# Optimization experiments

Measured on AMD Instinct MI355X. Metric: run time of the kernel, lower is better.

Reference implementation:

```python
import jax, jax.numpy as jnp
import numpy as np

DIM = 128
N_NODES = 100000
N_EDGES = 200000
M = 800000  # incidence pairs in each direction
L = 2
N_CLASS = 10


def setup_inputs() -> dict:
    key = jax.random.key(0)
    ks = jax.random.split(key, 8)
    s = 1.0 / np.sqrt(DIM)
    return {
        "node_x": jax.random.normal(ks[0], (N_NODES, DIM), jnp.float32),
        "nodes_map": jax.random.randint(ks[1], (M,), 0, N_NODES, jnp.int32),
        "edge_seg": jnp.sort(jax.random.randint(ks[2], (M,), 0, N_EDGES, jnp.int32)),
        "edges_map": jax.random.randint(ks[3], (M,), 0, N_EDGES, jnp.int32),
        "node_seg": jnp.sort(jax.random.randint(ks[4], (M,), 0, N_NODES, jnp.int32)),
        "num_edges": N_EDGES,
        "W_e": jax.random.normal(ks[5], (L, DIM, DIM), jnp.float32) * s,
        "b_e": jnp.zeros((L, DIM), jnp.float32),
        "g_e": jnp.ones((L, DIM), jnp.float32),
        "be_e": jnp.zeros((L, DIM), jnp.float32),
        "W_n": jax.random.normal(ks[6], (L, DIM, DIM), jnp.float32) * s,
        "b_n": jnp.zeros((L, DIM), jnp.float32),
        "g_n": jnp.ones((L, DIM), jnp.float32),
        "be_n": jnp.zeros((L, DIM), jnp.float32),
        "W_c": jax.random.normal(ks[7], (DIM, N_CLASS), jnp.float32) * s,
        "b_c": jnp.zeros((N_CLASS,), jnp.float32),
    }


def _seg_mean(x, seg, num_segments):
    # global_mean_pool: segment sum / count (count clamped to 1 for empty segments)
    s = jax.ops.segment_sum(x, seg, num_segments=num_segments)
    cnt = jax.ops.segment_sum(jnp.ones((x.shape[0],), x.dtype), seg, num_segments=num_segments)
    return s / jnp.maximum(cnt, 1.0)[:, None]


def _layernorm(x, g, b, eps=1e-5):
    m = jnp.mean(x, axis=-1, keepdims=True)
    v = jnp.mean(jnp.square(x - m), axis=-1, keepdims=True)
    return (x - m) * jax.lax.rsqrt(v + eps) * g + b


def reference(node_x, nodes_map, edge_seg, edges_map, node_seg, num_edges,
              W_e, b_e, g_e, be_e, W_n, b_n, g_n, be_n, W_c, b_c):
    n_nodes = node_x.shape[0]
    x = node_x  # in_drp = Dropout(0.0) is identity
    for i in range(W_e.shape[0]):
        # N2E: gather node feats per (edge, member) pair, mean-pool per hyperedge
        ex = _seg_mean(x[nodes_map], edge_seg, num_edges)          # [E, DIM]
        ex = jax.nn.relu(_layernorm(ex @ W_e[i] + b_e[i], g_e[i], be_e[i]))
        # E2N: gather edge feats per (node, incident-edge) pair, mean-pool per node
        x = _seg_mean(ex[edges_map], node_seg, n_nodes)            # [N, DIM]
        x = jax.nn.relu(_layernorm(x @ W_n[i] + b_n[i], g_n[i], be_n[i]))
    return jax.nn.log_softmax(x @ W_c + b_c, axis=-1)
```

## Files before the change

### kernel.cpp

```cpp
#include <hip/hip_runtime.h>
#include <hip/hip_bf16.h>

#define DIM 128

typedef __bf16 bf16x8 __attribute__((ext_vector_type(8)));
typedef float f32x4 __attribute__((ext_vector_type(4)));

static inline int cdiv(int a, int b) { return (a + b - 1) / b; }
static inline size_t align256(size_t x) { return (x + 255) & ~size_t(255); }

__device__ inline unsigned short f2bf(float f) {
    union { float f; unsigned int u; } v; v.f = f;
    unsigned int r = v.u + 0x7fff + ((v.u >> 16) & 1);
    return (unsigned short)(r >> 16);
}
__device__ inline unsigned int hb(float f) {
    return (__builtin_bit_cast(unsigned int, f) + 0x8000u) >> 16;
}

__global__ void setup_all_kernel(const int* __restrict__ segA, int mA, int nA,
                                 int* __restrict__ offA,
                                 const int* __restrict__ segB, int mB, int nB,
                                 int* __restrict__ offB,
                                 const float* __restrict__ xin,
                                 unsigned short* __restrict__ xout, int n4,
                                 const float* __restrict__ W_e,
                                 const float* __restrict__ W_n,
                                 unsigned short* __restrict__ wsw) {
    int gid = blockIdx.x * blockDim.x + threadIdx.x;

    if (gid < n4) {
        float4 v = ((const float4*)xin)[gid];
        ushort4 o;
        o.x = f2bf(v.x); o.y = f2bf(v.y); o.z = f2bf(v.z); o.w = f2bf(v.w);
        ((ushort4*)xout)[gid] = o;
    }

    if (gid <= nA) {
        int lo = 0, hi = mA;
        while (lo < hi) { int mid = (lo + hi) >> 1; if (segA[mid] < gid) lo = mid + 1; else hi = mid; }
        offA[gid] = lo;
    }
    int jj = gid - (nA + 1);
    if (jj >= 0 && jj <= nB) {
        int lo = 0, hi = mB;
        while (lo < hi) { int mid = (lo + hi) >> 1; if (segB[mid] < jj) lo = mid + 1; else hi = mid; }
        offB[jj] = lo;
    }

    if (gid < 8192) {
        int mi = gid >> 11;
        int e = gid & 2047;
        const float* W = (mi < 2) ? (W_e + (size_t)mi * DIM * DIM)
                                  : (W_n + (size_t)(mi - 2) * DIM * DIM);
        int t = e >> 9, n = (e >> 6) & 7, lane = e & 63;
        int q = lane >> 4, c = lane & 15;
        int k0 = t * 32 + q * 8, col = n * 16 + c;
        unsigned short vals[8];
#pragma unroll
        for (int j = 0; j < 8; ++j) vals[j] = f2bf(W[(size_t)(k0 + j) * DIM + col]);
        ushort4* dst = (ushort4*)(wsw + (size_t)gid * 8);
        dst[0] = make_ushort4(vals[0], vals[1], vals[2], vals[3]);
        dst[1] = make_ushort4(vals[4], vals[5], vals[6], vals[7]);
    }
}

__device__ inline void accum8(float* a, uint4 v) {
    unsigned int u[4] = {v.x, v.y, v.z, v.w};
#pragma unroll
    for (int i = 0; i < 4; ++i) {
        a[2 * i]     += __builtin_bit_cast(float, u[i] << 16);
        a[2 * i + 1] += __builtin_bit_cast(float, u[i]);
    }
}

__global__ __launch_bounds__(512)
void fused_pool_gemm_ln_relu_v8_kernel(const uint4* __restrict__ src,
                                       const int* __restrict__ map,
                                       const int* __restrict__ off,
                                       const unsigned short* __restrict__ Wsw,
                                       const float* __restrict__ b,
                                       const float* __restrict__ g,
                                       const float* __restrict__ be,
                                       unsigned short* __restrict__ Y,
                                       int nseg) {
    __shared__ bf16x8 wlds[2048];
    int tid = threadIdx.x;
    int w = tid >> 6, lane = tid & 63;
    int q = lane >> 4, c = lane & 15;

    {
        const uint4* gsrc = (const uint4*)Wsw;
        uint4* ldst = (uint4*)wlds;
#pragma unroll
        for (int i = 0; i < 4; ++i) ldst[tid + i * 512] = gsrc[tid + i * 512];
    }

    int blockbase = blockIdx.x * 128;
    int seg = min(blockbase + w * 16 + c, nseg - 1);
    int beg = off[seg], end = off[seg + 1];
    int e1 = max(end - 1, 0);
    unsigned r = (unsigned)map[min(beg, e1)];

    __syncthreads();

    float a[4][8];
#pragma unroll
    for (int t = 0; t < 4; ++t)
#pragma unroll
        for (int i = 0; i < 8; ++i) a[t][i] = 0.f;

    const char* sbase = (const char*)src;
    unsigned qb = (unsigned)(q << 4);
    for (int j = beg; j < end; ++j) {
        const char* p = sbase + ((r << 8) + qb);
        uint4 v0 = *(const uint4*)(p);
        uint4 v1 = *(const uint4*)(p + 64);
        uint4 v2 = *(const uint4*)(p + 128);
        uint4 v3 = *(const uint4*)(p + 192);
        unsigned rn = (unsigned)map[min(j + 1, e1)];
        accum8(a[0], v0);
        accum8(a[1], v1);
        accum8(a[2], v2);
        accum8(a[3], v3);
        r = rn;
    }

    float inv = 1.f / fmaxf((float)(end - beg), 1.f);
    bf16x8 af[4];
#pragma unroll
    for (int t = 0; t < 4; ++t) {
        uint4 o;
        o.x = hb(a[t][0] * inv) | (hb(a[t][1] * inv) << 16);
        o.y = hb(a[t][2] * inv) | (hb(a[t][3] * inv) << 16);
        o.z = hb(a[t][4] * inv) | (hb(a[t][5] * inv) << 16);
        o.w = hb(a[t][6] * inv) | (hb(a[t][7] * inv) << 16);
        af[t] = __builtin_bit_cast(bf16x8, o);
    }

    float bcol[8];
#pragma unroll
    for (int n = 0; n < 8; ++n) bcol[n] = b[n * 16 + c];

    f32x4 acc[8];
#pragma unroll
    for (int n = 0; n < 8; ++n) acc[n] = f32x4{bcol[n], bcol[n], bcol[n], bcol[n]};

#pragma unroll
    for (int n = 0; n < 8; ++n) {
        acc[n] = __builtin_amdgcn_mfma_f32_16x16x32_bf16(af[0], wlds[(0 * 8 + n) * 64 + lane], acc[n], 0, 0, 0);
        acc[n] = __builtin_amdgcn_mfma_f32_16x16x32_bf16(af[1], wlds[(1 * 8 + n) * 64 + lane], acc[n], 0, 0, 0);
        acc[n] = __builtin_amdgcn_mfma_f32_16x16x32_bf16(af[2], wlds[(2 * 8 + n) * 64 + lane], acc[n], 0, 0, 0);
        acc[n] = __builtin_amdgcn_mfma_f32_16x16x32_bf16(af[3], wlds[(3 * 8 + n) * 64 + lane], acc[n], 0, 0, 0);
    }

    float s1[4], s2[4];
#pragma unroll
    for (int j = 0; j < 4; ++j) {
        float t1 = 0.f, t2 = 0.f;
#pragma unroll
        for (int n = 0; n < 8; ++n) { float v = acc[n][j]; t1 += v; t2 = fmaf(v, v, t2); }
        s1[j] = t1; s2[j] = t2;
    }
#pragma unroll
    for (int o = 1; o < 16; o <<= 1)
#pragma unroll
        for (int j = 0; j < 4; ++j) {
            s1[j] += __shfl_xor(s1[j], o);
            s2[j] += __shfl_xor(s2[j], o);
        }

    float gcol[8], becol[8];
#pragma unroll
    for (int n = 0; n < 8; ++n) {
        int col = n * 16 + c;
        gcol[n] = g[col]; becol[n] = be[col];
    }

#pragma unroll
    for (int j = 0; j < 4; ++j) {
        int row = blockbase + w * 16 + q * 4 + j;
        if (row >= nseg) continue;
        float m = s1[j] * (1.f / DIM);
        float var = fmaf(-m, m, s2[j] * (1.f / DIM));
        float invs = rsqrtf(var + 1e-5f);
        unsigned short* yp = Y + (size_t)row * DIM + c;
#pragma unroll
        for (int n = 0; n < 8; ++n) {
            float d = acc[n][j] - m;
            float y = fmaxf(fmaf(d * invs, gcol[n], becol[n]), 0.f);
            unsigned int u = __builtin_bit_cast(unsigned int, y) + 0x8000u;
            yp[n * 16] = (unsigned short)(u >> 16);
        }
    }
}

#define CL_ROWS 4
__global__ __launch_bounds__(256)
void classifier_logsoftmax_v3_kernel(const uint4* __restrict__ X,
                                     const float* __restrict__ Wc,
                                     const float* __restrict__ bc,
                                     float* __restrict__ out, int nrows) {
    int w = threadIdx.x >> 6, lane = threadIdx.x & 63;
    int g = lane >> 4, c16 = lane & 15;
    int r0 = (blockIdx.x * 16 + w * 4 + g) * CL_ROWS;
    if (r0 >= nrows) return;

    float wc[8][10];
#pragma unroll
    for (int j = 0; j < 8; ++j)
#pragma unroll
        for (int c = 0; c < 10; ++c) wc[j][c] = Wc[(c16 * 8 + j) * 10 + c];
    float bcv[10];
#pragma unroll
    for (int c = 0; c < 10; ++c) bcv[c] = bc[c];

    int rend = min(r0 + CL_ROWS, nrows);
    for (int r = r0; r < rend; ++r) {
        uint4 v = X[(size_t)r * 16 + c16];
        float x[8];
        {
            unsigned int u[4] = {v.x, v.y, v.z, v.w};
#pragma unroll
            for (int i = 0; i < 4; ++i) {
                union { unsigned int ui; float f; } lo, hi;
                lo.ui = u[i] << 16;
                hi.ui = u[i] & 0xffff0000u;
                x[2 * i] = lo.f; x[2 * i + 1] = hi.f;
            }
        }
        float acc[10];
#pragma unroll
        for (int c = 0; c < 10; ++c) acc[c] = 0.f;
#pragma unroll
        for (int j = 0; j < 8; ++j)
#pragma unroll
            for (int c = 0; c < 10; ++c) acc[c] = fmaf(x[j], wc[j][c], acc[c]);

#pragma unroll
        for (int o = 1; o < 16; o <<= 1)
#pragma unroll
            for (int c = 0; c < 10; ++c) acc[c] += __shfl_xor(acc[c], o);

#pragma unroll
        for (int c = 0; c < 10; ++c) acc[c] += bcv[c];

        float mx = acc[0];
#pragma unroll
        for (int c = 1; c < 10; ++c) mx = fmaxf(mx, acc[c]);
        float se = 0.f;
#pragma unroll
        for (int c = 0; c < 10; ++c) se += expf(acc[c] - mx);
        float lse = mx + logf(se);

        float myv = 0.f;
#pragma unroll
        for (int c = 0; c < 10; ++c) myv = (c16 == c) ? acc[c] : myv;
        if (c16 < 10) out[(size_t)r * 10 + c16] = myv - lse;
    }
}

extern "C" void kernel_launch(void* const* d_in, const int* in_sizes, int n_in,
                              void* d_out, int out_size, void* d_ws, size_t ws_size,
                              hipStream_t stream) {
    const float* node_x    = (const float*)d_in[0];
    const int*   nodes_map = (const int*)d_in[1];
    const int*   edge_seg  = (const int*)d_in[2];
    const int*   edges_map = (const int*)d_in[3];
    const int*   node_seg  = (const int*)d_in[4];
    const float* W_e = (const float*)d_in[6];
    const float* b_e = (const float*)d_in[7];
    const float* g_e = (const float*)d_in[8];
    const float* be_e= (const float*)d_in[9];
    const float* W_n = (const float*)d_in[10];
    const float* b_n = (const float*)d_in[11];
    const float* g_n = (const float*)d_in[12];
    const float* be_n= (const float*)d_in[13];
    const float* W_c = (const float*)d_in[14];
    const float* b_c = (const float*)d_in[15];
    float* out = (float*)d_out;

    const int N = in_sizes[0] / DIM;
    const int M = in_sizes[1];
    const int E = 200000;
    const int L = in_sizes[6] / (DIM * DIM);

    char* ws = (char*)d_ws;
    int* edge_off = (int*)ws;           ws += align256((size_t)(E + 1) * sizeof(int));
    int* node_off = (int*)ws;           ws += align256((size_t)(N + 1) * sizeof(int));
    unsigned short* wsw = (unsigned short*)ws;      ws += align256((size_t)4 * 2048 * 8 * sizeof(unsigned short));
    unsigned short* node_xb = (unsigned short*)ws;  ws += align256((size_t)N * DIM * sizeof(unsigned short));
    unsigned short* exb = (unsigned short*)ws;      ws += align256((size_t)E * DIM * sizeof(unsigned short));
    unsigned short* xb  = (unsigned short*)ws;      ws += align256((size_t)N * DIM * sizeof(unsigned short));
    (void)ws_size;

    setup_all_kernel<<<cdiv(N * DIM / 4, 256), 256, 0, stream>>>(
        edge_seg, M, E, edge_off, node_seg, M, N, node_off,
        node_x, node_xb, N * DIM / 4, W_e, W_n, wsw);

    const unsigned short* xcur = node_xb;
    for (int i = 0; i < L; ++i) {
        fused_pool_gemm_ln_relu_v8_kernel<<<cdiv(E, 128), 512, 0, stream>>>(
            (const uint4*)xcur, nodes_map, edge_off, wsw + (size_t)i * 16384,
            b_e + i * DIM, g_e + i * DIM, be_e + i * DIM, exb, E);
        fused_pool_gemm_ln_relu_v8_kernel<<<cdiv(N, 128), 512, 0, stream>>>(
            (const uint4*)exb, edges_map, node_off, wsw + (size_t)(2 + i) * 16384,
            b_n + i * DIM, g_n + i * DIM, be_n + i * DIM, xb, N);
        xcur = xb;
    }

    classifier_logsoftmax_v3_kernel<<<cdiv(N, 16 * CL_ROWS), 256, 0, stream>>>(
        (const uint4*)xcur, W_c, b_c, out, N);
}
```

Measured before the change: 337.9 us.

## Gather rows with 16 lanes per row, unroll by four, bpermute into MFMA layout

Changes the gather-pool phase so that each group of 16 lanes covers one full 256-byte row with one 16-byte load per lane, giving coalesced row reads. Four segments are handled per wave in sequence, with the loop unrolled four entries deep using weighted FMAs that mask out-of-range tail entries, so more independent loads are in flight. The pooled results are then moved into the MFMA A-operand layout through ds_bpermute, and launch bounds request higher occupancy. In exchange it adds serial work over four segments per lane group, wasted loads in padded tail iterations, and shuffle overhead.

```diff
diff --git a/kernel.cpp b/kernel.cpp
--- a/kernel.cpp
+++ b/kernel.cpp
@@ -65,25 +65,25 @@
     }
 }
 
-__device__ inline void accum8(float* a, uint4 v) {
+__device__ inline void accum8s(float* a, uint4 v, float wt) {
     unsigned int u[4] = {v.x, v.y, v.z, v.w};
 #pragma unroll
     for (int i = 0; i < 4; ++i) {
-        a[2 * i]     += __builtin_bit_cast(float, u[i] << 16);
-        a[2 * i + 1] += __builtin_bit_cast(float, u[i]);
-    }
-}
-
-__global__ __launch_bounds__(512)
-void fused_pool_gemm_ln_relu_v8_kernel(const uint4* __restrict__ src,
-                                       const int* __restrict__ map,
-                                       const int* __restrict__ off,
-                                       const unsigned short* __restrict__ Wsw,
-                                       const float* __restrict__ b,
-                                       const float* __restrict__ g,
-                                       const float* __restrict__ be,
-                                       unsigned short* __restrict__ Y,
-                                       int nseg) {
+        a[2 * i]     = fmaf(wt, __builtin_bit_cast(float, u[i] << 16), a[2 * i]);
+        a[2 * i + 1] = fmaf(wt, __builtin_bit_cast(float, u[i]),       a[2 * i + 1]);
+    }
+}
+
+__global__ __launch_bounds__(512, 8)
+void fused_pool_gemm_ln_relu_v10_kernel(const uint4* __restrict__ src,
+                                        const int* __restrict__ map,
+                                        const int* __restrict__ off,
+                                        const unsigned short* __restrict__ Wsw,
+                                        const float* __restrict__ b,
+                                        const float* __restrict__ g,
+                                        const float* __restrict__ be,
+                                        unsigned short* __restrict__ Y,
+                                        int nseg) {
     __shared__ bf16x8 wlds[2048];
     int tid = threadIdx.x;
     int w = tid >> 6, lane = tid & 63;
@@ -97,44 +97,75 @@
     }
 
     int blockbase = blockIdx.x * 128;
-    int seg = min(blockbase + w * 16 + c, nseg - 1);
-    int beg = off[seg], end = off[seg + 1];
-    int e1 = max(end - 1, 0);
-    unsigned r = (unsigned)map[min(beg, e1)];
+    int wavebase = w * 16;
+
+    int begv[4], endv[4];
+#pragma unroll
+    for (int it = 0; it < 4; ++it) {
+        int sc = min(blockbase + wavebase + it * 4 + q, nseg - 1);
+        begv[it] = off[sc];
+        endv[it] = off[sc + 1];
+    }
 
     __syncthreads();
 
-    float a[4][8];
+    const char* sbase = (const char*)src;
+    unsigned cb = (unsigned)(c << 4);
+
+    unsigned afu[4][4];
 #pragma unroll
     for (int t = 0; t < 4; ++t)
 #pragma unroll
-        for (int i = 0; i < 8; ++i) a[t][i] = 0.f;
-
-    const char* sbase = (const char*)src;
-    unsigned qb = (unsigned)(q << 4);
-    for (int j = beg; j < end; ++j) {
-        const char* p = sbase + ((r << 8) + qb);
-        uint4 v0 = *(const uint4*)(p);
-        uint4 v1 = *(const uint4*)(p + 64);
-        uint4 v2 = *(const uint4*)(p + 128);
-        uint4 v3 = *(const uint4*)(p + 192);
-        unsigned rn = (unsigned)map[min(j + 1, e1)];
-        accum8(a[0], v0);
-        accum8(a[1], v1);
-        accum8(a[2], v2);
-        accum8(a[3], v3);
-        r = rn;
-    }
-
-    float inv = 1.f / fmaxf((float)(end - beg), 1.f);
+        for (int k = 0; k < 4; ++k) afu[t][k] = 0u;
+    int myit = (lane >> 2) & 3;
+
+#pragma unroll
+    for (int it = 0; it < 4; ++it) {
+        int beg = begv[it], end = endv[it];
+        int e1 = max(end - 1, 0);
+        float a[8] = {0.f, 0.f, 0.f, 0.f, 0.f, 0.f, 0.f, 0.f};
+        unsigned r0 = (unsigned)map[min(beg, e1)];
+        unsigned r1 = (unsigned)map[min(beg + 1, e1)];
+        unsigned r2 = (unsigned)map[min(beg + 2, e1)];
+        unsigned r3 = (unsigned)map[min(beg + 3, e1)];
+        for (int j = beg; j < end; j += 4) {
+            uint4 v0 = *(const uint4*)(sbase + ((r0 << 8) + cb));
+            uint4 v1 = *(const uint4*)(sbase + ((r1 << 8) + cb));
+            uint4 v2 = *(const uint4*)(sbase + ((r2 << 8) + cb));
+            uint4 v3 = *(const uint4*)(sbase + ((r3 << 8) + cb));
+            int jn = j + 4;
+            unsigned n0 = (unsigned)map[min(jn, e1)];
+            unsigned n1 = (unsigned)map[min(jn + 1, e1)];
+            unsigned n2 = (unsigned)map[min(jn + 2, e1)];
+            unsigned n3 = (unsigned)map[min(jn + 3, e1)];
+            accum8s(a, v0, 1.f);
+            accum8s(a, v1, (j + 1 < end) ? 1.f : 0.f);
+            accum8s(a, v2, (j + 2 < end) ? 1.f : 0.f);
+            accum8s(a, v3, (j + 3 < end) ? 1.f : 0.f);
+            r0 = n0; r1 = n1; r2 = n2; r3 = n3;
+        }
+        float inv = 1.f / fmaxf((float)(end - beg), 1.f);
+        unsigned P[4];
+        P[0] = hb(a[0] * inv) | (hb(a[1] * inv) << 16);
+        P[1] = hb(a[2] * inv) | (hb(a[3] * inv) << 16);
+        P[2] = hb(a[4] * inv) | (hb(a[5] * inv) << 16);
+        P[3] = hb(a[6] * inv) | (hb(a[7] * inv) << 16);
+        bool keep = (myit == it);
+#pragma unroll
+        for (int t = 0; t < 4; ++t) {
+            int srcb = ((((lane & 3) << 4) | ((lane >> 4) + 4 * t)) << 2);
+#pragma unroll
+            for (int k = 0; k < 4; ++k) {
+                int p = __builtin_amdgcn_ds_bpermute(srcb, (int)P[k]);
+                afu[t][k] = keep ? (unsigned)p : afu[t][k];
+            }
+        }
+    }
+
     bf16x8 af[4];
 #pragma unroll
     for (int t = 0; t < 4; ++t) {
-        uint4 o;
-        o.x = hb(a[t][0] * inv) | (hb(a[t][1] * inv) << 16);
-        o.y = hb(a[t][2] * inv) | (hb(a[t][3] * inv) << 16);
-        o.z = hb(a[t][4] * inv) | (hb(a[t][5] * inv) << 16);
-        o.w = hb(a[t][6] * inv) | (hb(a[t][7] * inv) << 16);
+        uint4 o = make_uint4(afu[t][0], afu[t][1], afu[t][2], afu[t][3]);
         af[t] = __builtin_bit_cast(bf16x8, o);
     }
 
@@ -300,10 +331,10 @@
 
     const unsigned short* xcur = node_xb;
     for (int i = 0; i < L; ++i) {
-        fused_pool_gemm_ln_relu_v8_kernel<<<cdiv(E, 128), 512, 0, stream>>>(
+        fused_pool_gemm_ln_relu_v10_kernel<<<cdiv(E, 128), 512, 0, stream>>>(
             (const uint4*)xcur, nodes_map, edge_off, wsw + (size_t)i * 16384,
             b_e + i * DIM, g_e + i * DIM, be_e + i * DIM, exb, E);
-        fused_pool_gemm_ln_relu_v8_kernel<<<cdiv(N, 128), 512, 0, stream>>>(
+        fused_pool_gemm_ln_relu_v10_kernel<<<cdiv(N, 128), 512, 0, stream>>>(
             (const uint4*)exb, edges_map, node_off, wsw + (size_t)(2 + i) * 16384,
             b_n + i * DIM, g_n + i * DIM, be_n + i * DIM, xb, N);
         xcur = xb;
```

New measurement: 474.7 us. 1.4x slower.
